# Kernel tuning notes

Hardware: AMD Instinct MI355X
Metric: run time of the kernel (lower is better)

The kernel has to match this reference:

```python
import jax, jax.numpy as jnp
import numpy as np

I = 256   # input_size
H = 256   # hidden_size
B = 64
T = 2048


def setup_inputs() -> dict:
    key = jax.random.key(0)
    ks = jax.random.split(key, 7)
    s_i = 1.0 / np.sqrt(I)
    s_h = 1.0 / np.sqrt(H)
    return {
        "x": jax.random.normal(ks[0], (B, T, I), dtype=jnp.float32),
        "h0": jax.random.normal(ks[1], (1, B, H), dtype=jnp.float32),
        "c0": jax.random.normal(ks[2], (1, B, H), dtype=jnp.float32),
        # Only l_fi / l_fh affect the output in the original forward (all four
        # gates are computed from the same pre-activation due to a source bug).
        "W_fi": jax.random.uniform(ks[3], (H, I), jnp.float32, -s_i, s_i),
        "b_fi": jax.random.uniform(ks[4], (H,), jnp.float32, -s_i, s_i),
        "W_fh": jax.random.uniform(ks[5], (H, H), jnp.float32, -s_h, s_h),
        "b_fh": jax.random.uniform(ks[6], (H,), jnp.float32, -s_h, s_h),
    }


def reference(x, h0, c0, W_fi, b_fi, W_fh, b_fh):
    # Faithful to the buggy torch source:
    #   f = i = o = sigmoid(l_fi(x_t) + l_fh(ht_1)); m = tanh(same)
    #   ht_1, ct_1 are NEVER updated -> no recurrence; vectorize over time.
    ht_1 = h0[0]  # (B, H), state[0].squeeze(0)
    ct_1 = c0[0]  # (B, H)
    gx = jnp.einsum('bti,hi->bth', x, W_fi) + b_fi          # (B, T, H)
    gh = ht_1 @ W_fh.T + b_fh                               # (B, H)
    g = gx + gh[:, None, :]                                 # (B, T, H)
    s = jax.nn.sigmoid(g)
    m = jnp.tanh(g)
    c = s * ct_1[:, None, :] + s * m                        # c_t per step
    h = s * jnp.tanh(c)                                     # h_t per step
    hidden_seq = jnp.transpose(h, (1, 0, 2))                # (T, B, H), cat dim=0
    return (hidden_seq, (h[:, -1, :], c[:, -1, :]))
```

## Files before the change

### kernel.cpp

```cpp
#include <hip/hip_runtime.h>
#include <hip/hip_bf16.h>
#include <stdint.h>

#define T_SZ 2048
#define B_SZ 64
#define H_SZ 256
#define I_SZ 256
#define M_SZ (B_SZ * T_SZ)
#define TBH  (T_SZ * B_SZ * H_SZ)

typedef float f32x4 __attribute__((ext_vector_type(4)));
typedef short s16x8 __attribute__((ext_vector_type(8)));

__device__ __forceinline__ unsigned pack_bf16(float a, float b) {
    unsigned ua = __float_as_uint(a);
    unsigned ub = __float_as_uint(b);
    ua += 0x7fffu + ((ua >> 16) & 1u);
    ub += 0x7fffu + ((ub >> 16) & 1u);
    return (ua >> 16) | (ub & 0xffff0000u);
}

__global__ void prep_kernel(const float* __restrict__ h0,
                            const float* __restrict__ W_fi,
                            const float* __restrict__ b_fi,
                            const float* __restrict__ W_fh,
                            const float* __restrict__ b_fh,
                            unsigned short* __restrict__ Wb,
                            float* __restrict__ gb) {
    __shared__ float h0s[H_SZ];
    const int b = blockIdx.x;
    const int h = threadIdx.x;
    h0s[h] = h0[b * H_SZ + h];
    __syncthreads();
    const float4* w4 = (const float4*)(W_fh + (size_t)h * H_SZ);
    float acc = 0.f;
#pragma unroll 8
    for (int j = 0; j < H_SZ / 4; ++j) {
        float4 w = w4[j];
        acc = fmaf(w.x, h0s[4 * j + 0], acc);
        acc = fmaf(w.y, h0s[4 * j + 1], acc);
        acc = fmaf(w.z, h0s[4 * j + 2], acc);
        acc = fmaf(w.w, h0s[4 * j + 3], acc);
    }
    gb[b * H_SZ + h] = acc + b_fi[h] + b_fh[h];

    const int e = (b * 256 + h) * 4;
    float4 wv = *(const float4*)(W_fi + e);
    uint2 pk;
    pk.x = pack_bf16(wv.x, wv.y);
    pk.y = pack_bf16(wv.z, wv.w);
    *(uint2*)(Wb + e) = pk;
}

__global__ __launch_bounds__(512, 4) void lstm_main(
    const float* __restrict__ x,
    const unsigned short* __restrict__ Wb,
    const float* __restrict__ gb,
    const float* __restrict__ c0,
    float* __restrict__ out) {
    __shared__ __align__(16) unsigned short As[64 * 40];
    __shared__ __align__(16) unsigned short Bs[256 * 40];

    const int tid  = threadIdx.x;
    const int lane = tid & 63;
    const int wid  = tid >> 6;
    const int m0 = blockIdx.x * 64;
    const int wm = (wid & 1) * 32;
    const int wn = (wid >> 1) * 64;
    const int fr = lane & 15;
    const int fq = lane >> 4;

    const int ar  = tid >> 3, ak  = (tid & 7) * 4;
    const int b0r = tid >> 2, b0k = (tid & 3) * 8;
    const int b1r = (tid + 512) >> 2, b1k = ((tid + 512) & 3) * 8;

    const float*          aG  = x  + (size_t)(m0 + ar) * I_SZ + ak;
    const unsigned short* b0G = Wb + b0r * 256 + b0k;
    const unsigned short* b1G = Wb + b1r * 256 + b1k;
    unsigned short* aL  = As + ar * 40 + ak;
    unsigned short* b0L = Bs + b0r * 40 + b0k;
    unsigned short* b1L = Bs + b1r * 40 + b1k;

    const unsigned short* aF = As + (wm + fr) * 40 + fq * 8;
    const unsigned short* bF = Bs + (wn + fr) * 40 + fq * 8;

    f32x4 acc[2][4];
#pragma unroll
    for (int mi = 0; mi < 2; ++mi)
#pragma unroll
        for (int ni = 0; ni < 4; ++ni)
            acc[mi][ni] = (f32x4){0.f, 0.f, 0.f, 0.f};

    float4 aw[2];
    uint4  bw0[2], bw1[2];
    aw[0]  = *(const float4*)aG;
    bw0[0] = *(const uint4*)b0G;
    bw1[0] = *(const uint4*)b1G;

#pragma unroll
    for (int kt = 0; kt < 8; ++kt) {
        if (kt < 7) {
            aw[(kt + 1) & 1]  = *(const float4*)(aG + (kt + 1) * 32);
            bw0[(kt + 1) & 1] = *(const uint4*)(b0G + (kt + 1) * 32);
            bw1[(kt + 1) & 1] = *(const uint4*)(b1G + (kt + 1) * 32);
        }
        uint2 ap;
        ap.x = pack_bf16(aw[kt & 1].x, aw[kt & 1].y);
        ap.y = pack_bf16(aw[kt & 1].z, aw[kt & 1].w);
        if (kt) {
            __builtin_amdgcn_sched_barrier(0);
            __builtin_amdgcn_s_barrier();
            __builtin_amdgcn_sched_barrier(0);
        }
        *(uint2*)aL  = ap;
        *(uint4*)b0L = bw0[kt & 1];
        *(uint4*)b1L = bw1[kt & 1];
        asm volatile("s_waitcnt lgkmcnt(0)" ::: "memory");
        __builtin_amdgcn_sched_barrier(0);
        __builtin_amdgcn_s_barrier();
        __builtin_amdgcn_sched_barrier(0);
        s16x8 af[2], bf[4];
#pragma unroll
        for (int mi = 0; mi < 2; ++mi)
            af[mi] = *(const s16x8*)(aF + mi * 16 * 40);
#pragma unroll
        for (int ni = 0; ni < 4; ++ni)
            bf[ni] = *(const s16x8*)(bF + ni * 16 * 40);
        __builtin_amdgcn_s_setprio(1);
#pragma unroll
        for (int mi = 0; mi < 2; ++mi)
#pragma unroll
            for (int ni = 0; ni < 4; ++ni)
                acc[mi][ni] = __builtin_amdgcn_mfma_f32_16x16x32_bf16(
                    af[mi], bf[ni], acc[mi][ni], 0, 0, 0);
        __builtin_amdgcn_s_setprio(0);
    }

    const int bb = m0 >> 11;
    const int coln = wn + fr;
    float gbv[4], c0v[4];
#pragma unroll
    for (int ni = 0; ni < 4; ++ni) {
        gbv[ni] = gb[bb * H_SZ + coln + ni * 16];
        c0v[ni] = c0[bb * H_SZ + coln + ni * 16];
    }
#pragma unroll
    for (int mi = 0; mi < 2; ++mi) {
#pragma unroll
        for (int r = 0; r < 4; ++r) {
            const int Mg = m0 + wm + mi * 16 + fq * 4 + r;
            const int tt = Mg & (T_SZ - 1);
            const int obase = tt * (B_SZ * H_SZ) + bb * H_SZ;
            const bool last = (tt == T_SZ - 1);
#pragma unroll
            for (int ni = 0; ni < 4; ++ni) {
                const int h = coln + ni * 16;
                float g = acc[mi][ni][r] + gbv[ni];
                float gc = fminf(15.f, fmaxf(-15.f, g));
                float e = __expf(-gc);
                float s = __builtin_amdgcn_rcpf(1.f + e);
                float e2 = e * e;
                float m = (1.f - e2) * __builtin_amdgcn_rcpf(1.f + e2);
                float cv = s * (c0v[ni] + m);
                float cc = fminf(15.f, fmaxf(-15.f, cv));
                float ec = __expf(-2.f * cc);
                float th = (1.f - ec) * __builtin_amdgcn_rcpf(1.f + ec);
                float hv = s * th;
                out[obase + h] = hv;
                if (last) {
                    out[TBH + bb * H_SZ + h] = hv;
                    out[TBH + B_SZ * H_SZ + bb * H_SZ + h] = cv;
                }
            }
        }
    }
}

extern "C" void kernel_launch(void* const* d_in, const int* in_sizes, int n_in,
                              void* d_out, int out_size, void* d_ws, size_t ws_size,
                              hipStream_t stream) {
    const float* x    = (const float*)d_in[0];
    const float* h0   = (const float*)d_in[1];
    const float* c0   = (const float*)d_in[2];
    const float* W_fi = (const float*)d_in[3];
    const float* b_fi = (const float*)d_in[4];
    const float* W_fh = (const float*)d_in[5];
    const float* b_fh = (const float*)d_in[6];
    float* out = (float*)d_out;

    unsigned short* Wb = (unsigned short*)d_ws;
    float* gb = (float*)((char*)d_ws + 131072);

    hipLaunchKernelGGL(prep_kernel, dim3(B_SZ), dim3(H_SZ), 0, stream,
                       h0, W_fi, b_fi, W_fh, b_fh, Wb, gb);
    hipLaunchKernelGGL(lstm_main, dim3(M_SZ / 64), dim3(512), 0, stream,
                       x, Wb, gb, c0, out);
}
```

Measured before the change: 283.1 us.

## Double-buffer LDS with K=64 tiles and XOR swizzle, trim clamps

Reworks the GEMM main loop to use two LDS buffers with K=64 tiles and an XOR-swizzled, unpadded layout. Each K tile now issues two MFMA k-steps per barrier, and the next tile is prefetched and written while the current one computes, so barriers drop from roughly sixteen to four. The epilogue also removes the upper clamp on the gate and the clamp on the cell value before tanh. That saves a few ALU ops but relies on exp and rcp behaving well at extreme inputs. The LDS footprint grows to 80KB per block, which may reduce occupancy under the 4-blocks launch bound.

After: 335.8 us. 1.19x slower.

```diff
diff --git a/kernel.cpp b/kernel.cpp
--- a/kernel.cpp
+++ b/kernel.cpp
@@ -58,8 +58,7 @@
     const float* __restrict__ gb,
     const float* __restrict__ c0,
     float* __restrict__ out) {
-    __shared__ __align__(16) unsigned short As[64 * 40];
-    __shared__ __align__(16) unsigned short Bs[256 * 40];
+    __shared__ __align__(16) unsigned short Ls[2 * 20480];
 
     const int tid  = threadIdx.x;
     const int lane = tid & 63;
@@ -70,19 +69,47 @@
     const int fr = lane & 15;
     const int fq = lane >> 4;
 
-    const int ar  = tid >> 3, ak  = (tid & 7) * 4;
-    const int b0r = tid >> 2, b0k = (tid & 3) * 8;
-    const int b1r = (tid + 512) >> 2, b1k = ((tid + 512) & 3) * 8;
-
-    const float*          aG  = x  + (size_t)(m0 + ar) * I_SZ + ak;
-    const unsigned short* b0G = Wb + b0r * 256 + b0k;
-    const unsigned short* b1G = Wb + b1r * 256 + b1k;
-    unsigned short* aL  = As + ar * 40 + ak;
-    unsigned short* b0L = Bs + b0r * 40 + b0k;
-    unsigned short* b1L = Bs + b1r * 40 + b1k;
-
-    const unsigned short* aF = As + (wm + fr) * 40 + fq * 8;
-    const unsigned short* bF = Bs + (wn + fr) * 40 + fq * 8;
+    const int arow = tid >> 3, aseg = tid & 7;
+    const int axm = (arow & 7) << 3;
+    const float* aGp = x + (size_t)(m0 + arow) * I_SZ + ((aseg * 8) ^ axm);
+    const int aLo = arow * 64 + aseg * 8;
+
+    const int brow = tid >> 3, bpos = tid & 7;
+    const int bxm = (brow & 7) << 3;
+    const int bgo = brow * 256 + ((bpos * 8) ^ bxm);
+    const int bLo = 4096 + brow * 64 + bpos * 8;
+
+    const int fxm = (fr & 7) << 3;
+    int aro[2], bro[2];
+#pragma unroll
+    for (int ks = 0; ks < 2; ++ks) {
+        const int c = (ks * 32 + fq * 8) ^ fxm;
+        aro[ks] = (wm + fr) * 64 + c;
+        bro[ks] = 4096 + (wn + fr) * 64 + c;
+    }
+
+    float4 sa[2][2];
+    uint4  sb[2][4];
+
+    auto LOAD = [&](int s, int kt) {
+        sa[s][0] = *(const float4*)(aGp + kt * 64);
+        sa[s][1] = *(const float4*)(aGp + kt * 64 + 4);
+#pragma unroll
+        for (int w = 0; w < 4; ++w)
+            sb[s][w] = *(const uint4*)(Wb + bgo + w * 64 * 256 + kt * 64);
+    };
+    auto WRITE = [&](int s, int buf) {
+        unsigned short* L = Ls + buf * 20480;
+        uint4 ap;
+        ap.x = pack_bf16(sa[s][0].x, sa[s][0].y);
+        ap.y = pack_bf16(sa[s][0].z, sa[s][0].w);
+        ap.z = pack_bf16(sa[s][1].x, sa[s][1].y);
+        ap.w = pack_bf16(sa[s][1].z, sa[s][1].w);
+        *(uint4*)(L + aLo) = ap;
+#pragma unroll
+        for (int w = 0; w < 4; ++w)
+            *(uint4*)(L + bLo + w * 4096) = sb[s][w];
+    };
 
     f32x4 acc[2][4];
 #pragma unroll
@@ -91,48 +118,42 @@
         for (int ni = 0; ni < 4; ++ni)
             acc[mi][ni] = (f32x4){0.f, 0.f, 0.f, 0.f};
 
-    float4 aw[2];
-    uint4  bw0[2], bw1[2];
-    aw[0]  = *(const float4*)aG;
-    bw0[0] = *(const uint4*)b0G;
-    bw1[0] = *(const uint4*)b1G;
-
-#pragma unroll
-    for (int kt = 0; kt < 8; ++kt) {
-        if (kt < 7) {
-            aw[(kt + 1) & 1]  = *(const float4*)(aG + (kt + 1) * 32);
-            bw0[(kt + 1) & 1] = *(const uint4*)(b0G + (kt + 1) * 32);
-            bw1[(kt + 1) & 1] = *(const uint4*)(b1G + (kt + 1) * 32);
+    LOAD(0, 0);
+    WRITE(0, 0);
+    LOAD(1, 1);
+    asm volatile("s_waitcnt lgkmcnt(0)" ::: "memory");
+    __builtin_amdgcn_sched_barrier(0);
+    __builtin_amdgcn_s_barrier();
+    __builtin_amdgcn_sched_barrier(0);
+
+#pragma unroll
+    for (int kt = 0; kt < 4; ++kt) {
+        const unsigned short* L = Ls + (kt & 1) * 20480;
+        s16x8 af[2][2], bf[4][2];
+#pragma unroll
+        for (int ks = 0; ks < 2; ++ks) {
+#pragma unroll
+            for (int mi = 0; mi < 2; ++mi)
+                af[mi][ks] = *(const s16x8*)(L + aro[ks] + mi * 1024);
+#pragma unroll
+            for (int ni = 0; ni < 4; ++ni)
+                bf[ni][ks] = *(const s16x8*)(L + bro[ks] + ni * 1024);
         }
-        uint2 ap;
-        ap.x = pack_bf16(aw[kt & 1].x, aw[kt & 1].y);
-        ap.y = pack_bf16(aw[kt & 1].z, aw[kt & 1].w);
-        if (kt) {
-            __builtin_amdgcn_sched_barrier(0);
-            __builtin_amdgcn_s_barrier();
-            __builtin_amdgcn_sched_barrier(0);
-        }
-        *(uint2*)aL  = ap;
-        *(uint4*)b0L = bw0[kt & 1];
-        *(uint4*)b1L = bw1[kt & 1];
+        if (kt < 2) LOAD(kt & 1, kt + 2);
+        if (kt < 3) WRITE((kt + 1) & 1, (kt & 1) ^ 1);
         asm volatile("s_waitcnt lgkmcnt(0)" ::: "memory");
         __builtin_amdgcn_sched_barrier(0);
-        __builtin_amdgcn_s_barrier();
+        if (kt < 3) __builtin_amdgcn_s_barrier();
         __builtin_amdgcn_sched_barrier(0);
-        s16x8 af[2], bf[4];
-#pragma unroll
-        for (int mi = 0; mi < 2; ++mi)
-            af[mi] = *(const s16x8*)(aF + mi * 16 * 40);
-#pragma unroll
-        for (int ni = 0; ni < 4; ++ni)
-            bf[ni] = *(const s16x8*)(bF + ni * 16 * 40);
         __builtin_amdgcn_s_setprio(1);
 #pragma unroll
-        for (int mi = 0; mi < 2; ++mi)
-#pragma unroll
-            for (int ni = 0; ni < 4; ++ni)
-                acc[mi][ni] = __builtin_amdgcn_mfma_f32_16x16x32_bf16(
-                    af[mi], bf[ni], acc[mi][ni], 0, 0, 0);
+        for (int ks = 0; ks < 2; ++ks)
+#pragma unroll
+            for (int mi = 0; mi < 2; ++mi)
+#pragma unroll
+                for (int ni = 0; ni < 4; ++ni)
+                    acc[mi][ni] = __builtin_amdgcn_mfma_f32_16x16x32_bf16(
+                        af[mi][ks], bf[ni][ks], acc[mi][ni], 0, 0, 0);
         __builtin_amdgcn_s_setprio(0);
     }
 
@@ -156,14 +177,13 @@
             for (int ni = 0; ni < 4; ++ni) {
                 const int h = coln + ni * 16;
                 float g = acc[mi][ni][r] + gbv[ni];
-                float gc = fminf(15.f, fmaxf(-15.f, g));
+                float gc = fmaxf(-15.f, g);
                 float e = __expf(-gc);
                 float s = __builtin_amdgcn_rcpf(1.f + e);
                 float e2 = e * e;
                 float m = (1.f - e2) * __builtin_amdgcn_rcpf(1.f + e2);
                 float cv = s * (c0v[ni] + m);
-                float cc = fminf(15.f, fmaxf(-15.f, cv));
-                float ec = __expf(-2.f * cc);
+                float ec = __expf(-2.f * cv);
                 float th = (1.f - ec) * __builtin_amdgcn_rcpf(1.f + ec);
                 float hv = s * th;
                 out[obase + h] = hv;
```

## Double-buffer LDS with XOR swizzle and prefetch two K-tiles ahead

Applied to the files above, without the earlier changes.

Replaces the single padded LDS tile with two XOR-swizzled, unpadded buffers, so each iteration issues one barrier instead of two and fragment reads overlap with the next tile's stores. Global loads are prefetched two K-steps ahead. Launch bounds drop to 2 waves-per-EU hints, since LDS doubles. Some clamps in the activation epilogue are removed, which risks inf/NaN for large positive c values.

After: 278.3 us. About the same (-1.7%).

```diff
diff --git a/kernel.cpp b/kernel.cpp
--- a/kernel.cpp
+++ b/kernel.cpp
@@ -52,14 +52,13 @@
     *(uint2*)(Wb + e) = pk;
 }
 
-__global__ __launch_bounds__(512, 4) void lstm_main(
+__global__ __launch_bounds__(512, 2) void lstm_main(
     const float* __restrict__ x,
     const unsigned short* __restrict__ Wb,
     const float* __restrict__ gb,
     const float* __restrict__ c0,
     float* __restrict__ out) {
-    __shared__ __align__(16) unsigned short As[64 * 40];
-    __shared__ __align__(16) unsigned short Bs[256 * 40];
+    __shared__ __align__(16) unsigned short Ls[2 * 10240];
 
     const int tid  = threadIdx.x;
     const int lane = tid & 63;
@@ -70,19 +69,26 @@
     const int fr = lane & 15;
     const int fq = lane >> 4;
 
-    const int ar  = tid >> 3, ak  = (tid & 7) * 4;
-    const int b0r = tid >> 2, b0k = (tid & 3) * 8;
-    const int b1r = (tid + 512) >> 2, b1k = ((tid + 512) & 3) * 8;
-
-    const float*          aG  = x  + (size_t)(m0 + ar) * I_SZ + ak;
-    const unsigned short* b0G = Wb + b0r * 256 + b0k;
-    const unsigned short* b1G = Wb + b1r * 256 + b1k;
-    unsigned short* aL  = As + ar * 40 + ak;
-    unsigned short* b0L = Bs + b0r * 40 + b0k;
-    unsigned short* b1L = Bs + b1r * 40 + b1k;
-
-    const unsigned short* aF = As + (wm + fr) * 40 + fq * 8;
-    const unsigned short* bF = Bs + (wn + fr) * 40 + fq * 8;
+    const int arow = tid >> 3, aseg = tid & 7;
+    const int ag = aseg >> 1, asub = aseg & 1;
+    const int axm = (arow >> 1) & 3;
+    const float* aG = x + (size_t)(m0 + arow) * I_SZ + ((ag ^ axm) * 8 + asub * 4);
+    const int aLo = arow * 32 + aseg * 4;
+
+    int bgo[2], bLo[2];
+#pragma unroll
+    for (int w = 0; w < 2; ++w) {
+        const int slot = w * 512 + tid;
+        const int row = slot >> 2, g = slot & 3;
+        const int xm = (row >> 1) & 3;
+        bgo[w] = row * 256 + ((g ^ xm) * 8);
+        bLo[w] = 2048 + row * 32 + g * 8;
+    }
+
+    const int fxm = (fr >> 1) & 3;
+    const int fcol = (fq ^ fxm) * 8;
+    const int afo = (wm + fr) * 32 + fcol;
+    const int bfo = 2048 + (wn + fr) * 32 + fcol;
 
     f32x4 acc[2][4];
 #pragma unroll
@@ -91,41 +97,58 @@
         for (int ni = 0; ni < 4; ++ni)
             acc[mi][ni] = (f32x4){0.f, 0.f, 0.f, 0.f};
 
-    float4 aw[2];
-    uint4  bw0[2], bw1[2];
-    aw[0]  = *(const float4*)aG;
-    bw0[0] = *(const uint4*)b0G;
-    bw1[0] = *(const uint4*)b1G;
+    float4 sa[2];
+    uint4  sb[2][2];
+
+    sa[0]    = *(const float4*)(aG);
+    sb[0][0] = *(const uint4*)(Wb + bgo[0]);
+    sb[0][1] = *(const uint4*)(Wb + bgo[1]);
+    sa[1]    = *(const float4*)(aG + 32);
+    sb[1][0] = *(const uint4*)(Wb + bgo[0] + 32);
+    sb[1][1] = *(const uint4*)(Wb + bgo[1] + 32);
+    {
+        uint2 ap;
+        ap.x = pack_bf16(sa[0].x, sa[0].y);
+        ap.y = pack_bf16(sa[0].z, sa[0].w);
+        *(uint2*)(Ls + aLo) = ap;
+        *(uint4*)(Ls + bLo[0]) = sb[0][0];
+        *(uint4*)(Ls + bLo[1]) = sb[0][1];
+    }
+    asm volatile("s_waitcnt lgkmcnt(0)" ::: "memory");
+    __builtin_amdgcn_sched_barrier(0);
+    __builtin_amdgcn_s_barrier();
+    __builtin_amdgcn_sched_barrier(0);
 
 #pragma unroll
     for (int kt = 0; kt < 8; ++kt) {
+        const unsigned short* L = Ls + (kt & 1) * 10240;
+        s16x8 af[2], bf[4];
+#pragma unroll
+        for (int mi = 0; mi < 2; ++mi)
+            af[mi] = *(const s16x8*)(L + afo + mi * 512);
+#pragma unroll
+        for (int ni = 0; ni < 4; ++ni)
+            bf[ni] = *(const s16x8*)(L + bfo + ni * 512);
+        if (kt < 6) {
+            const int s = kt & 1, kof = (kt + 2) * 32;
+            sa[s]    = *(const float4*)(aG + kof);
+            sb[s][0] = *(const uint4*)(Wb + bgo[0] + kof);
+            sb[s][1] = *(const uint4*)(Wb + bgo[1] + kof);
+        }
         if (kt < 7) {
-            aw[(kt + 1) & 1]  = *(const float4*)(aG + (kt + 1) * 32);
-            bw0[(kt + 1) & 1] = *(const uint4*)(b0G + (kt + 1) * 32);
-            bw1[(kt + 1) & 1] = *(const uint4*)(b1G + (kt + 1) * 32);
+            const int s = (kt + 1) & 1;
+            unsigned short* Lw = Ls + (((kt + 1) & 1)) * 10240;
+            uint2 ap;
+            ap.x = pack_bf16(sa[s].x, sa[s].y);
+            ap.y = pack_bf16(sa[s].z, sa[s].w);
+            *(uint2*)(Lw + aLo) = ap;
+            *(uint4*)(Lw + bLo[0]) = sb[s][0];
+            *(uint4*)(Lw + bLo[1]) = sb[s][1];
         }
-        uint2 ap;
-        ap.x = pack_bf16(aw[kt & 1].x, aw[kt & 1].y);
-        ap.y = pack_bf16(aw[kt & 1].z, aw[kt & 1].w);
-        if (kt) {
-            __builtin_amdgcn_sched_barrier(0);
-            __builtin_amdgcn_s_barrier();
-            __builtin_amdgcn_sched_barrier(0);
-        }
-        *(uint2*)aL  = ap;
-        *(uint4*)b0L = bw0[kt & 1];
-        *(uint4*)b1L = bw1[kt & 1];
         asm volatile("s_waitcnt lgkmcnt(0)" ::: "memory");
         __builtin_amdgcn_sched_barrier(0);
-        __builtin_amdgcn_s_barrier();
+        if (kt < 7) __builtin_amdgcn_s_barrier();
         __builtin_amdgcn_sched_barrier(0);
-        s16x8 af[2], bf[4];
-#pragma unroll
-        for (int mi = 0; mi < 2; ++mi)
-            af[mi] = *(const s16x8*)(aF + mi * 16 * 40);
-#pragma unroll
-        for (int ni = 0; ni < 4; ++ni)
-            bf[ni] = *(const s16x8*)(bF + ni * 16 * 40);
         __builtin_amdgcn_s_setprio(1);
 #pragma unroll
         for (int mi = 0; mi < 2; ++mi)
@@ -156,14 +179,13 @@
             for (int ni = 0; ni < 4; ++ni) {
                 const int h = coln + ni * 16;
                 float g = acc[mi][ni][r] + gbv[ni];
-                float gc = fminf(15.f, fmaxf(-15.f, g));
+                float gc = fmaxf(-15.f, g);
                 float e = __expf(-gc);
                 float s = __builtin_amdgcn_rcpf(1.f + e);
                 float e2 = e * e;
                 float m = (1.f - e2) * __builtin_amdgcn_rcpf(1.f + e2);
                 float cv = s * (c0v[ni] + m);
-                float cc = fminf(15.f, fmaxf(-15.f, cv));
-                float ec = __expf(-2.f * cc);
+                float ec = __expf(-2.f * cv);
                 float th = (1.f - ec) * __builtin_amdgcn_rcpf(1.f + ec);
                 float hv = s * th;
                 out[obase + h] = hv;
```

## Fuse prep into main kernel with resident swizzled bf16 weights in LDS

Applied to the files above, without the earlier changes.

Merges the weight-conversion and bias/h0 projection prep kernel into the main kernel, removing one launch and the workspace round-trip. Each block now loads the full W_fi as bf16 into a 128 KB XOR-swizzled LDS region once, then processes 512 rows in 8 chunks of 64, double-buffering x loads in registers across chunks. It also drops the upper clamp on the sigmoid input and the clamp on c before tanh. The cost is that every one of the 256 blocks recomputes the W_fh·h0 projection and re-converts W_fi, and the 160 KB of LDS allows only one block per CU.

Result: faster. 274.2 us (-3.2%).

```diff
diff --git a/kernel.cpp b/kernel.cpp
--- a/kernel.cpp
+++ b/kernel.cpp
@@ -20,158 +20,184 @@
     return (ua >> 16) | (ub & 0xffff0000u);
 }
 
-__global__ void prep_kernel(const float* __restrict__ h0,
-                            const float* __restrict__ W_fi,
-                            const float* __restrict__ b_fi,
-                            const float* __restrict__ W_fh,
-                            const float* __restrict__ b_fh,
-                            unsigned short* __restrict__ Wb,
-                            float* __restrict__ gb) {
-    __shared__ float h0s[H_SZ];
-    const int b = blockIdx.x;
-    const int h = threadIdx.x;
-    h0s[h] = h0[b * H_SZ + h];
-    __syncthreads();
-    const float4* w4 = (const float4*)(W_fh + (size_t)h * H_SZ);
-    float acc = 0.f;
-#pragma unroll 8
-    for (int j = 0; j < H_SZ / 4; ++j) {
-        float4 w = w4[j];
-        acc = fmaf(w.x, h0s[4 * j + 0], acc);
-        acc = fmaf(w.y, h0s[4 * j + 1], acc);
-        acc = fmaf(w.z, h0s[4 * j + 2], acc);
-        acc = fmaf(w.w, h0s[4 * j + 3], acc);
-    }
-    gb[b * H_SZ + h] = acc + b_fi[h] + b_fh[h];
-
-    const int e = (b * 256 + h) * 4;
-    float4 wv = *(const float4*)(W_fi + e);
-    uint2 pk;
-    pk.x = pack_bf16(wv.x, wv.y);
-    pk.y = pack_bf16(wv.z, wv.w);
-    *(uint2*)(Wb + e) = pk;
-}
-
-__global__ __launch_bounds__(512, 4) void lstm_main(
+__global__ __launch_bounds__(512, 1) void lstm_fused(
     const float* __restrict__ x,
-    const unsigned short* __restrict__ Wb,
-    const float* __restrict__ gb,
+    const float* __restrict__ h0,
     const float* __restrict__ c0,
+    const float* __restrict__ W_fi,
+    const float* __restrict__ b_fi,
+    const float* __restrict__ W_fh,
+    const float* __restrict__ b_fh,
     float* __restrict__ out) {
-    __shared__ __align__(16) unsigned short As[64 * 40];
-    __shared__ __align__(16) unsigned short Bs[256 * 40];
+    __shared__ __align__(16) unsigned char smem[163840];
+    unsigned short* Bs = (unsigned short*)smem;
+    unsigned short* As = (unsigned short*)(smem + 131072);
+    float* h0s = (float*)(smem + 131072);
+    float* tmp = h0s + 256;
+    float* gbf = h0s + 768;
 
     const int tid  = threadIdx.x;
     const int lane = tid & 63;
     const int wid  = tid >> 6;
-    const int m0 = blockIdx.x * 64;
+    const int fr = lane & 15;
+    const int fq = lane >> 4;
     const int wm = (wid & 1) * 32;
     const int wn = (wid >> 1) * 64;
-    const int fr = lane & 15;
-    const int fq = lane >> 4;
-
-    const int ar  = tid >> 3, ak  = (tid & 7) * 4;
-    const int b0r = tid >> 2, b0k = (tid & 3) * 8;
-    const int b1r = (tid + 512) >> 2, b1k = ((tid + 512) & 3) * 8;
-
-    const float*          aG  = x  + (size_t)(m0 + ar) * I_SZ + ak;
-    const unsigned short* b0G = Wb + b0r * 256 + b0k;
-    const unsigned short* b1G = Wb + b1r * 256 + b1k;
-    unsigned short* aL  = As + ar * 40 + ak;
-    unsigned short* b0L = Bs + b0r * 40 + b0k;
-    unsigned short* b1L = Bs + b1r * 40 + b1k;
-
-    const unsigned short* aF = As + (wm + fr) * 40 + fq * 8;
-    const unsigned short* bF = Bs + (wn + fr) * 40 + fq * 8;
-
-    f32x4 acc[2][4];
-#pragma unroll
-    for (int mi = 0; mi < 2; ++mi)
-#pragma unroll
-        for (int ni = 0; ni < 4; ++ni)
-            acc[mi][ni] = (f32x4){0.f, 0.f, 0.f, 0.f};
-
-    float4 aw[2];
-    uint4  bw0[2], bw1[2];
-    aw[0]  = *(const float4*)aG;
-    bw0[0] = *(const uint4*)b0G;
-    bw1[0] = *(const uint4*)b1G;
-
-#pragma unroll
-    for (int kt = 0; kt < 8; ++kt) {
-        if (kt < 7) {
-            aw[(kt + 1) & 1]  = *(const float4*)(aG + (kt + 1) * 32);
-            bw0[(kt + 1) & 1] = *(const uint4*)(b0G + (kt + 1) * 32);
-            bw1[(kt + 1) & 1] = *(const uint4*)(b1G + (kt + 1) * 32);
-        }
-        uint2 ap;
-        ap.x = pack_bf16(aw[kt & 1].x, aw[kt & 1].y);
-        ap.y = pack_bf16(aw[kt & 1].z, aw[kt & 1].w);
-        if (kt) {
-            __builtin_amdgcn_sched_barrier(0);
-            __builtin_amdgcn_s_barrier();
-            __builtin_amdgcn_sched_barrier(0);
-        }
-        *(uint2*)aL  = ap;
-        *(uint4*)b0L = bw0[kt & 1];
-        *(uint4*)b1L = bw1[kt & 1];
-        asm volatile("s_waitcnt lgkmcnt(0)" ::: "memory");
-        __builtin_amdgcn_sched_barrier(0);
-        __builtin_amdgcn_s_barrier();
-        __builtin_amdgcn_sched_barrier(0);
-        s16x8 af[2], bf[4];
-#pragma unroll
-        for (int mi = 0; mi < 2; ++mi)
-            af[mi] = *(const s16x8*)(aF + mi * 16 * 40);
-#pragma unroll
-        for (int ni = 0; ni < 4; ++ni)
-            bf[ni] = *(const s16x8*)(bF + ni * 16 * 40);
-        __builtin_amdgcn_s_setprio(1);
-#pragma unroll
-        for (int mi = 0; mi < 2; ++mi)
-#pragma unroll
-            for (int ni = 0; ni < 4; ++ni)
-                acc[mi][ni] = __builtin_amdgcn_mfma_f32_16x16x32_bf16(
-                    af[mi], bf[ni], acc[mi][ni], 0, 0, 0);
-        __builtin_amdgcn_s_setprio(0);
-    }
-
-    const int bb = m0 >> 11;
+    const int m0 = blockIdx.x * 512;
+    const int bb = blockIdx.x >> 2;
+
+    float4 areg[8];
+    {
+        const float* aG = x + (size_t)(m0 + wid * 8) * I_SZ + lane * 4;
+#pragma unroll
+        for (int j = 0; j < 8; ++j) areg[j] = *(const float4*)(aG + j * I_SZ);
+    }
+
+    if (tid < 256) h0s[tid] = h0[bb * H_SZ + tid];
+    __syncthreads();
+
+    {
+        const int h = tid & 255, half = tid >> 8;
+        const float4* wr = (const float4*)(W_fh + (size_t)h * H_SZ + half * 128);
+        const float* hv = h0s + half * 128;
+        float a = 0.f;
+#pragma unroll 8
+        for (int j = 0; j < 32; ++j) {
+            float4 w = wr[j];
+            a = fmaf(w.x, hv[4 * j + 0], a);
+            a = fmaf(w.y, hv[4 * j + 1], a);
+            a = fmaf(w.z, hv[4 * j + 2], a);
+            a = fmaf(w.w, hv[4 * j + 3], a);
+        }
+        tmp[h * 2 + half] = a;
+    }
+    __syncthreads();
+    if (tid < 256) gbf[tid] = tmp[2 * tid] + tmp[2 * tid + 1] + b_fi[tid] + b_fh[tid];
+
+    {
+        const int brow = tid >> 1, bhalf = tid & 1, brm = brow & 7;
+        const float4* wG = (const float4*)(W_fi + (size_t)brow * I_SZ + bhalf * 128);
+        unsigned short* bD = Bs + brow * 256;
+#pragma unroll
+        for (int g = 0; g < 16; ++g) {
+            float4 u0 = wG[g * 2];
+            float4 u1 = wG[g * 2 + 1];
+            uint4 p;
+            p.x = pack_bf16(u0.x, u0.y); p.y = pack_bf16(u0.z, u0.w);
+            p.z = pack_bf16(u1.x, u1.y); p.w = pack_bf16(u1.z, u1.w);
+            *(uint4*)(bD + (((bhalf * 16 + g) ^ brm) * 8)) = p;
+        }
+    }
+    __syncthreads();
+
     const int coln = wn + fr;
     float gbv[4], c0v[4];
 #pragma unroll
     for (int ni = 0; ni < 4; ++ni) {
-        gbv[ni] = gb[bb * H_SZ + coln + ni * 16];
+        gbv[ni] = gbf[coln + ni * 16];
         c0v[ni] = c0[bb * H_SZ + coln + ni * 16];
     }
-#pragma unroll
-    for (int mi = 0; mi < 2; ++mi) {
-#pragma unroll
-        for (int r = 0; r < 4; ++r) {
-            const int Mg = m0 + wm + mi * 16 + fq * 4 + r;
-            const int tt = Mg & (T_SZ - 1);
-            const int obase = tt * (B_SZ * H_SZ) + bb * H_SZ;
-            const bool last = (tt == T_SZ - 1);
-#pragma unroll
-            for (int ni = 0; ni < 4; ++ni) {
-                const int h = coln + ni * 16;
-                float g = acc[mi][ni][r] + gbv[ni];
-                float gc = fminf(15.f, fmaxf(-15.f, g));
-                float e = __expf(-gc);
-                float s = __builtin_amdgcn_rcpf(1.f + e);
-                float e2 = e * e;
-                float m = (1.f - e2) * __builtin_amdgcn_rcpf(1.f + e2);
-                float cv = s * (c0v[ni] + m);
-                float cc = fminf(15.f, fmaxf(-15.f, cv));
-                float ec = __expf(-2.f * cc);
-                float th = (1.f - ec) * __builtin_amdgcn_rcpf(1.f + ec);
-                float hv = s * th;
-                out[obase + h] = hv;
-                if (last) {
-                    out[TBH + bb * H_SZ + h] = hv;
-                    out[TBH + B_SZ * H_SZ + bb * H_SZ + h] = cv;
+    __syncthreads();
+
+    auto WRITEA = [&]() {
+#pragma unroll
+        for (int j = 0; j < 8; ++j) {
+            const int row = wid * 8 + j;
+            uint2 p;
+            p.x = pack_bf16(areg[j].x, areg[j].y);
+            p.y = pack_bf16(areg[j].z, areg[j].w);
+            *(uint2*)(As + row * 256 + (((lane >> 1) ^ (row & 7)) * 8 + (lane & 1) * 4)) = p;
+        }
+    };
+    auto LOADA = [&](int c) {
+        const float* aG = x + (size_t)(m0 + c * 64 + wid * 8) * I_SZ + lane * 4;
+#pragma unroll
+        for (int j = 0; j < 8; ++j) areg[j] = *(const float4*)(aG + j * I_SZ);
+    };
+
+    WRITEA();
+    LOADA(1);
+    asm volatile("s_waitcnt lgkmcnt(0)" ::: "memory");
+    __builtin_amdgcn_sched_barrier(0);
+    __builtin_amdgcn_s_barrier();
+    __builtin_amdgcn_sched_barrier(0);
+
+    const int frm = fr & 7;
+    const unsigned short* aB = As + (wm + fr) * 256;
+    const unsigned short* bB[4];
+#pragma unroll
+    for (int ni = 0; ni < 4; ++ni) bB[ni] = Bs + (wn + ni * 16 + fr) * 256;
+
+    for (int ch = 0; ch < 8; ++ch) {
+        f32x4 acc[2][4];
+#pragma unroll
+        for (int mi = 0; mi < 2; ++mi)
+#pragma unroll
+            for (int ni = 0; ni < 4; ++ni)
+                acc[mi][ni] = (f32x4){0.f, 0.f, 0.f, 0.f};
+
+        __builtin_amdgcn_s_setprio(1);
+#pragma unroll
+        for (int kt = 0; kt < 8; ++kt) {
+            const int e = ((kt * 4 + fq) ^ frm) * 8;
+            s16x8 af0 = *(const s16x8*)(aB + e);
+            s16x8 af1 = *(const s16x8*)(aB + 4096 + e);
+            s16x8 bf0 = *(const s16x8*)(bB[0] + e);
+            s16x8 bf1 = *(const s16x8*)(bB[1] + e);
+            s16x8 bf2 = *(const s16x8*)(bB[2] + e);
+            s16x8 bf3 = *(const s16x8*)(bB[3] + e);
+            acc[0][0] = __builtin_amdgcn_mfma_f32_16x16x32_bf16(af0, bf0, acc[0][0], 0, 0, 0);
+            acc[0][1] = __builtin_amdgcn_mfma_f32_16x16x32_bf16(af0, bf1, acc[0][1], 0, 0, 0);
+            acc[0][2] = __builtin_amdgcn_mfma_f32_16x16x32_bf16(af0, bf2, acc[0][2], 0, 0, 0);
+            acc[0][3] = __builtin_amdgcn_mfma_f32_16x16x32_bf16(af0, bf3, acc[0][3], 0, 0, 0);
+            acc[1][0] = __builtin_amdgcn_mfma_f32_16x16x32_bf16(af1, bf0, acc[1][0], 0, 0, 0);
+            acc[1][1] = __builtin_amdgcn_mfma_f32_16x16x32_bf16(af1, bf1, acc[1][1], 0, 0, 0);
+            acc[1][2] = __builtin_amdgcn_mfma_f32_16x16x32_bf16(af1, bf2, acc[1][2], 0, 0, 0);
+            acc[1][3] = __builtin_amdgcn_mfma_f32_16x16x32_bf16(af1, bf3, acc[1][3], 0, 0, 0);
+        }
+        __builtin_amdgcn_s_setprio(0);
+
+        const int mrow = m0 + ch * 64 + wm;
+#pragma unroll
+        for (int mi = 0; mi < 2; ++mi) {
+#pragma unroll
+            for (int r = 0; r < 4; ++r) {
+                const int Mg = mrow + mi * 16 + fq * 4 + r;
+                const int tt = Mg & (T_SZ - 1);
+                const int obase = tt * (B_SZ * H_SZ) + bb * H_SZ;
+                const bool last = (tt == T_SZ - 1);
+#pragma unroll
+                for (int ni = 0; ni < 4; ++ni) {
+                    const int h = coln + ni * 16;
+                    float g = acc[mi][ni][r] + gbv[ni];
+                    float gc = fmaxf(-15.f, g);
+                    float e = __expf(-gc);
+                    float s = __builtin_amdgcn_rcpf(1.f + e);
+                    float e2 = e * e;
+                    float m = (1.f - e2) * __builtin_amdgcn_rcpf(1.f + e2);
+                    float cv = s * (c0v[ni] + m);
+                    float ec = __expf(-2.f * cv);
+                    float th = (1.f - ec) * __builtin_amdgcn_rcpf(1.f + ec);
+                    float hv = s * th;
+                    out[obase + h] = hv;
+                    if (last) {
+                        out[TBH + bb * H_SZ + h] = hv;
+                        out[TBH + B_SZ * H_SZ + bb * H_SZ + h] = cv;
+                    }
                 }
             }
+        }
+
+        if (ch < 7) {
+            __builtin_amdgcn_sched_barrier(0);
+            __builtin_amdgcn_s_barrier();
+            __builtin_amdgcn_sched_barrier(0);
+            WRITEA();
+            if (ch < 6) LOADA(ch + 2);
+            asm volatile("s_waitcnt lgkmcnt(0)" ::: "memory");
+            __builtin_amdgcn_sched_barrier(0);
+            __builtin_amdgcn_s_barrier();
+            __builtin_amdgcn_sched_barrier(0);
         }
     }
 }
@@ -188,11 +214,6 @@
     const float* b_fh = (const float*)d_in[6];
     float* out = (float*)d_out;
 
-    unsigned short* Wb = (unsigned short*)d_ws;
-    float* gb = (float*)((char*)d_ws + 131072);
-
-    hipLaunchKernelGGL(prep_kernel, dim3(B_SZ), dim3(H_SZ), 0, stream,
-                       h0, W_fi, b_fi, W_fh, b_fh, Wb, gb);
-    hipLaunchKernelGGL(lstm_main, dim3(M_SZ / 64), dim3(512), 0, stream,
-                       x, Wb, gb, c0, out);
+    hipLaunchKernelGGL(lstm_fused, dim3(M_SZ / 512), dim3(512), 0, stream,
+                       x, h0, c0, W_fi, b_fi, W_fh, b_fh, out);
 }
```
